# Kernel optimization log

Hardware: AMD Instinct MI355X
Metric: run time of the kernel (lower is better)

Reference implementation:

```python
import jax, jax.numpy as jnp
import numpy as np

EPS = 1e-5

def _linear(x, w, b):
    # torch nn.Linear convention: w is [out, in]
    return jnp.einsum('...i,oi->...o', x, w) + b

def _l2_normalize(x, axis=-1):
    n = jnp.sqrt(jnp.sum(x * x, axis=axis, keepdims=True))
    return x / jnp.maximum(n, 1e-12)

def _online_softmax_scan(sim):
    # sim: [B, H, L]. Running max m_t and running sum s_t = sum_{i<=t} exp(sim_i - m_t)
    def combine(a, b):
        ma, sa = a
        mb, sb = b
        m = jnp.maximum(ma, mb)
        s = sa * jnp.exp(ma - m) + sb * jnp.exp(mb - m)
        return m, s
    m_scan, s_scan = jax.lax.associative_scan(combine, (sim, jnp.ones_like(sim)), axis=2)
    return m_scan, s_scan


def setup_inputs() -> dict:
    key = jax.random.key(0)
    ks = jax.random.split(key, 8)
    B, L, D = 2, 2048, 256
    H, h = 8, 32
    s = 1.0 / np.sqrt(D)
    inp = {
        'x': jax.random.normal(ks[0], (B, L, D), jnp.float32),
        'wq_w': jax.random.normal(ks[1], (D, D), jnp.float32) * s,
        'wq_b': jnp.zeros((D,), jnp.float32),
        'wk_w': jax.random.normal(ks[2], (D, D), jnp.float32) * s,
        'wk_b': jnp.zeros((D,), jnp.float32),
        'wv_w': jax.random.normal(ks[3], (D, D), jnp.float32) * s,
        'wv_b': jnp.zeros((D,), jnp.float32),
        'wo_w': jax.random.normal(ks[4], (D, D), jnp.float32) * s,
        'wo_b': jnp.zeros((D,), jnp.float32),
        'wg_w': jax.random.normal(ks[5], (1, h * h), jnp.float32) * (1.0 / np.sqrt(h * h)),
        'wg_b': jnp.zeros((1,), jnp.float32),
        'kv_norm_scale': jnp.ones((1, H, 1, h, h), jnp.float32),
        'qk_norm_scale': jnp.full((1, H, 1), 1.0 / np.sqrt(h), jnp.float32),
    }
    return inp


def reference(x, wq_w, wq_b, wk_w, wk_b, wv_w, wv_b, wo_w, wo_b,
              wg_w, wg_b, kv_norm_scale, qk_norm_scale):
    B, L, D = x.shape
    H, h = kv_norm_scale.shape[1], kv_norm_scale.shape[3]

    q = _linear(x, wq_w, wq_b).reshape(B, L, H, h).transpose(0, 2, 1, 3)  # bhld
    k = _linear(x, wk_w, wk_b).reshape(B, L, H, h).transpose(0, 2, 1, 3)
    v = _linear(x, wv_w, wv_b).reshape(B, L, H, h).transpose(0, 2, 1, 3)

    sim = jnp.einsum('bhld,bhld->bhl', q, k) * qk_norm_scale  # [B,H,L]

    k = _l2_normalize(k)
    v = _l2_normalize(v)

    # outer-product KV state per position: [B,H,L,h,h]
    Z = jnp.einsum('bhld,bhle->bhlde', v, k) * kv_norm_scale

    # gating: squared ReLU of linear over flattened h*h features
    gate_inputs = Z.reshape(B, H, L, h * h)
    gates_logits = jnp.einsum('bhli,oi->bhlo', gate_inputs, wg_w) + wg_b  # [B,H,L,1]
    gates = jnp.square(jax.nn.relu(gates_logits)) + EPS
    gates = gates[..., None]  # [B,H,L,1,1]
    gated_Z = gates * Z

    # associative scans along L
    m_scan, s_scan = _online_softmax_scan(sim)        # [B,H,L]
    Z_scan = jnp.cumsum(gated_Z, axis=2)              # [B,H,L,h,h]
    g_scan = jnp.cumsum(gates, axis=2)                # [B,H,L,1,1]

    softmax_weights = (jnp.exp(sim - m_scan) / (s_scan + EPS))[..., None, None]
    gated_weights = Z_scan / (g_scan + EPS)
    attn_weights = gated_weights * (1.0 + jax.nn.silu(softmax_weights))

    ctxt = jnp.einsum('bhld,bhlde->bhle', q, attn_weights)
    ctxt = ctxt.transpose(0, 2, 1, 3).reshape(B, L, D)
    return _linear(ctxt, wo_w, wo_b)
```

## Files before the change

kernel.cpp:

```cpp
#include <hip/hip_runtime.h>
#include <math.h>

#define EPSV 1e-5f

static constexpr int Ls = 2048, Hh = 8;
static constexpr int NCH = 64, T = 32;

typedef unsigned short u16;
using frag  = __attribute__((ext_vector_type(8))) short;
using f32x4 = __attribute__((ext_vector_type(4))) float;

__device__ __forceinline__ void split_bf16(float v, u16& hi, u16& lo) {
    const unsigned u = __float_as_uint(v);
    hi = (u16)(u >> 16);
    const float hf = __uint_as_float((unsigned)hi << 16);
    lo = (u16)(__float_as_uint(v - hf) >> 16);
}

__device__ __forceinline__ unsigned pk2(u16 a, u16 b) {
    return (unsigned)a | ((unsigned)b << 16);
}

__device__ __forceinline__ void split8(const float4& a, const float4& b,
                                       uint4& hi, uint4& lo) {
    u16 h[8], l[8];
    const float f[8] = {a.x, a.y, a.z, a.w, b.x, b.y, b.z, b.w};
#pragma unroll
    for (int i = 0; i < 8; ++i) split_bf16(f[i], h[i], l[i]);
    hi = make_uint4(pk2(h[0], h[1]), pk2(h[2], h[3]), pk2(h[4], h[5]), pk2(h[6], h[7]));
    lo = make_uint4(pk2(l[0], l[1]), pk2(l[2], l[3]), pk2(l[4], l[5]), pk2(l[6], l[7]));
}

__global__ __launch_bounds__(256) void qkv_fused(
    const float* __restrict__ x,
    const float* __restrict__ wq, const float* __restrict__ wk, const float* __restrict__ wv,
    const float* __restrict__ bq, const float* __restrict__ bk, const float* __restrict__ bv,
    const float* __restrict__ wg_w, const float* __restrict__ wg_b,
    const float* __restrict__ kvs, const float* __restrict__ qks,
    float* __restrict__ qh, float* __restrict__ kh, float* __restrict__ vh,
    float* __restrict__ simG, float* __restrict__ gG,
    float* __restrict__ ZcT, float* __restrict__ mT, float* __restrict__ sT,
    float* __restrict__ gTt)
{
    constexpr int LDK = 40;
    constexpr int LDT = 66;
    __shared__ __align__(16) float smemf[8960];
    __shared__ float lsim[2][32], lg2[2][32];

    u16* As_hi = (u16*)smemf;
    u16* As_lo = As_hi + 1280;
    u16* Wst   = As_lo + 1280;
    float* Qt = smemf;
    float* Kt = Qt + 32 * LDT;
    float* Vt = Kt + 32 * LDT;
    float* wkS = smemf + 6336;

    const int tid = threadIdx.x;
    const int mt = blockIdx.x, nt = blockIdx.y;
    const int m0 = mt * 32, ncol0 = nt * 64;
    const int bidx = m0 >> 11, lg = m0 & (Ls - 1);
    const int cg = lg >> 5;
    const int wave = tid >> 6, lane = tid & 63;
    const int l15 = lane & 15, quad = lane >> 4;
    const int srow = tid >> 2, sk = (tid & 3) * 8;
    const int rf = wave & 1, cfp = wave >> 1;

    const float* Wsrc[3] = {wq, wk, wv};
    f32x4 acc[3][2] = {};

    float4 ca0, ca1, cw0[3], cw1[3];
    if (tid < 128) {
        ca0 = *(const float4*)&x[(size_t)(m0 + srow) * 256 + 0 + sk];
        ca1 = *(const float4*)&x[(size_t)(m0 + srow) * 256 + 0 + sk + 4];
    }
#pragma unroll
    for (int w = 0; w < 3; ++w) {
        cw0[w] = *(const float4*)&Wsrc[w][(size_t)(ncol0 + srow) * 256 + 0 + sk];
        cw1[w] = *(const float4*)&Wsrc[w][(size_t)(ncol0 + srow) * 256 + 0 + sk + 4];
    }

#pragma unroll
    for (int kk = 0; kk < 8; ++kk) {
        __syncthreads();
        {
            uint4 hi, lo;
            if (tid < 128) {
                split8(ca0, ca1, hi, lo);
                *(uint4*)&As_hi[srow * LDK + sk] = hi;
                *(uint4*)&As_lo[srow * LDK + sk] = lo;
            }
#pragma unroll
            for (int w = 0; w < 3; ++w) {
                split8(cw0[w], cw1[w], hi, lo);
                *(uint4*)&Wst[w * 5120 + srow * LDK + sk] = hi;
                *(uint4*)&Wst[w * 5120 + 2560 + srow * LDK + sk] = lo;
            }
        }
        __syncthreads();

        if (kk < 7) {
            const int k0n = (kk + 1) * 32;
            if (tid < 128) {
                ca0 = *(const float4*)&x[(size_t)(m0 + srow) * 256 + k0n + sk];
                ca1 = *(const float4*)&x[(size_t)(m0 + srow) * 256 + k0n + sk + 4];
            }
#pragma unroll
            for (int w = 0; w < 3; ++w) {
                cw0[w] = *(const float4*)&Wsrc[w][(size_t)(ncol0 + srow) * 256 + k0n + sk];
                cw1[w] = *(const float4*)&Wsrc[w][(size_t)(ncol0 + srow) * 256 + k0n + sk + 4];
            }
        }

        const frag ah = *(const frag*)&As_hi[(rf * 16 + l15) * LDK + quad * 8];
        const frag al = *(const frag*)&As_lo[(rf * 16 + l15) * LDK + quad * 8];
#pragma unroll
        for (int w = 0; w < 3; ++w)
#pragma unroll
            for (int cf = 0; cf < 2; ++cf) {
                const u16* bp = &Wst[w * 5120 + ((cfp * 2 + cf) * 16 + l15) * LDK + quad * 8];
                const frag bh = *(const frag*)bp;
                const frag bl = *(const frag*)(bp + 2560);
                acc[w][cf] = __builtin_amdgcn_mfma_f32_16x16x32_bf16(ah, bh, acc[w][cf], 0, 0, 0);
                acc[w][cf] = __builtin_amdgcn_mfma_f32_16x16x32_bf16(ah, bl, acc[w][cf], 0, 0, 0);
                acc[w][cf] = __builtin_amdgcn_mfma_f32_16x16x32_bf16(al, bh, acc[w][cf], 0, 0, 0);
            }
    }
    __syncthreads();

    {
        float* tiles[3] = {Qt, Kt, Vt};
        const float* biases[3] = {bq, bk, bv};
#pragma unroll
        for (int w = 0; w < 3; ++w)
#pragma unroll
            for (int cf = 0; cf < 2; ++cf) {
                const int col = (cfp * 2 + cf) * 16 + l15;
                const float bias = biases[w][ncol0 + col];
#pragma unroll
                for (int r = 0; r < 4; ++r) {
                    const int m = rf * 16 + quad * 4 + r;
                    tiles[w][m * LDT + col] = acc[w][cf][r] + bias;
                }
            }
        for (int i = tid; i < 2048; i += 256) {
            const int h = i >> 10, de = i & 1023;
            wkS[h * 1024 + de] = wg_w[de] * kvs[(nt * 2 + h) * 1024 + de];
        }
    }
    __syncthreads();

    {
        const int task = tid >> 2, sub = tid & 3;
        const int h = task >> 5, l = task & 31;
        const int cb = h * 32, e0 = sub * 8;
        float ksum = 0.f, vsum = 0.f, qk = 0.f;
#pragma unroll
        for (int e = e0; e < e0 + 8; ++e) {
            const float kv = Kt[l * LDT + cb + e];
            const float vv = Vt[l * LDT + cb + e];
            const float qv = Qt[l * LDT + cb + e];
            ksum = fmaf(kv, kv, ksum);
            vsum = fmaf(vv, vv, vsum);
            qk = fmaf(qv, kv, qk);
        }
        ksum += __shfl_xor(ksum, 1); ksum += __shfl_xor(ksum, 2);
        vsum += __shfl_xor(vsum, 1); vsum += __shfl_xor(vsum, 2);
        qk   += __shfl_xor(qk, 1);   qk   += __shfl_xor(qk, 2);
        const float kscale = 1.f / fmaxf(sqrtf(ksum), 1e-12f);
        const float vscale = 1.f / fmaxf(sqrtf(vsum), 1e-12f);
#pragma unroll
        for (int e = e0; e < e0 + 8; ++e) {
            Kt[l * LDT + cb + e] *= kscale;
            Vt[l * LDT + cb + e] *= vscale;
        }
        if (sub == 0) {
            const float sim = qk * qks[nt * 2 + h];
            lsim[h][l] = sim;
            simG[(size_t)(bidx * 8 + nt * 2 + h) * Ls + lg + l] = sim;
        }
    }
    __syncthreads();

    {
        const float* tl[3] = {Qt, Kt, Vt};
        float* gl[3] = {qh, kh, vh};
#pragma unroll
        for (int arr = 0; arr < 3; ++arr)
#pragma unroll
            for (int it = 0; it < 4; ++it) {
                const int idx = it * 512 + tid * 2;
                const int l = idx >> 6, col = idx & 63;
                const int h = col >> 5, e = col & 31;
                float2 v;
                v.x = tl[arr][l * LDT + h * 32 + e];
                v.y = tl[arr][l * LDT + h * 32 + e + 1];
                *(float2*)&gl[arr][(size_t)(bidx * 8 + nt * 2 + h) * 65536 +
                                   (size_t)(lg + l) * 32 + e] = v;
            }
    }

    {
        const int task = tid >> 2, sub = tid & 3;
        const int h = task >> 5, l = task & 31;
        float vreg[32];
#pragma unroll 8
        for (int d = 0; d < 32; ++d) vreg[d] = Vt[l * LDT + h * 32 + d];
        float u = 0.f;
        const int e0 = sub * 8;
#pragma unroll
        for (int e = e0; e < e0 + 8; ++e) {
            float s = 0.f;
#pragma unroll 8
            for (int d = 0; d < 32; ++d)
                s = fmaf(vreg[d], wkS[h * 1024 + d * 32 + e], s);
            u = fmaf(s, Kt[l * LDT + h * 32 + e], u);
        }
        u += __shfl_xor(u, 1);
        u += __shfl_xor(u, 2);
        if (sub == 0) {
            const float r = fmaxf(u + wg_b[0], 0.f);
            const float g = r * r + EPSV;
            lg2[h][l] = g;
            gG[(size_t)(bidx * 8 + nt * 2 + h) * Ls + lg + l] = g;
        }
    }
    __syncthreads();

    {
        const int d = tid >> 3, e0 = (tid & 7) * 4;
#pragma unroll
        for (int h = 0; h < 2; ++h) {
            float z0 = 0.f, z1 = 0.f, z2 = 0.f, z3 = 0.f;
#pragma unroll 8
            for (int l = 0; l < 32; ++l) {
                const float gv = lg2[h][l] * Vt[l * LDT + h * 32 + d];
                z0 = fmaf(gv, Kt[l * LDT + h * 32 + e0 + 0], z0);
                z1 = fmaf(gv, Kt[l * LDT + h * 32 + e0 + 1], z1);
                z2 = fmaf(gv, Kt[l * LDT + h * 32 + e0 + 2], z2);
                z3 = fmaf(gv, Kt[l * LDT + h * 32 + e0 + 3], z3);
            }
            const int bhg = bidx * 8 + nt * 2 + h;
            float4 zv; zv.x = z0; zv.y = z1; zv.z = z2; zv.w = z3;
            *(float4*)&ZcT[((size_t)bhg * NCH + cg) * 1024 + d * 32 + e0] = zv;
        }
    }

    if (wave < 2 && lane < 32) {
        const int h = wave;
        float m = lsim[h][lane], s = 1.f, g = lg2[h][lane];
#pragma unroll
        for (int off = 16; off; off >>= 1) {
            const float mo = __shfl_xor(m, off);
            const float so = __shfl_xor(s, off);
            const float mn = fmaxf(m, mo);
            s = s * __expf(m - mn) + so * __expf(mo - mn);
            m = mn;
            g += __shfl_xor(g, off);
        }
        if (lane == 0) {
            const int bhg = bidx * 8 + nt * 2 + h;
            mT[bhg * NCH + cg] = m;
            sT[bhg * NCH + cg] = s;
            gTt[bhg * NCH + cg] = g;
        }
    }
}

__global__ __launch_bounds__(256) void prefix_kernel(
    float* __restrict__ Zc, float* __restrict__ mT, float* __restrict__ sT,
    float* __restrict__ gTt,
    const float* __restrict__ kvs, float* __restrict__ aW, float* __restrict__ bW,
    int* __restrict__ flagW)
{
    const int bh = blockIdx.x, seg = blockIdx.y;
    const int tid = threadIdx.x;
    const int el = seg * 256 + tid;
    float* Zb = Zc + (size_t)bh * NCH * 1024 + el;

    float v[NCH];
#pragma unroll
    for (int i = 0; i < NCH; ++i) v[i] = Zb[(size_t)i * 1024];
    float run = 0.f;
#pragma unroll
    for (int i = 0; i < NCH; ++i) {
        const float t = v[i];
        Zb[(size_t)i * 1024] = run;
        run += t;
    }

    if (seg == 0 && tid < 64) {
        float m = mT[bh * NCH + tid], s = sT[bh * NCH + tid], g = gTt[bh * NCH + tid];
#pragma unroll
        for (int off = 1; off < 64; off <<= 1) {
            const float mo = __shfl_up(m, off);
            const float so = __shfl_up(s, off);
            const float go = __shfl_up(g, off);
            if (tid >= off) {
                const float mn = fmaxf(m, mo);
                s = s * __expf(m - mn) + so * __expf(mo - mn);
                m = mn;
                g += go;
            }
        }
        float me = __shfl_up(m, 1), se = __shfl_up(s, 1), ge = __shfl_up(g, 1);
        if (tid == 0) { me = -1e30f; se = 0.f; ge = 0.f; }
        mT[bh * NCH + tid] = me;
        sT[bh * NCH + tid] = se;
        gTt[bh * NCH + tid] = ge;
    }

    if (bh == 0 && seg == 3) {
        const int h = tid >> 5, e = tid & 31;
        const float* K = kvs + h * 1024;
        const float k00 = K[0];
        int ok = (k00 != 0.0f);
        for (int d = 0; d < 32; ++d) {
            const float lhs = K[d * 32 + e] * k00;
            const float rhs = K[d * 32] * K[e];
            const float diff = fabsf(lhs - rhs);
            if (diff > 1e-6f * fmaxf(fmaxf(fabsf(lhs), fabsf(rhs)), 1e-20f)) ok = 0;
        }
        aW[h * 32 + e] = K[e * 32];
        bW[h * 32 + e] = (k00 != 0.0f) ? K[e] / k00 : 0.f;
        const int allok = __syncthreads_and(ok);
        if (tid == 0) flagW[0] = allok;
    }
}

__global__ __launch_bounds__(1024) void chunk_out_kernel(
    const float* __restrict__ qh, const float* __restrict__ knG, const float* __restrict__ vnG,
    const float* __restrict__ simG, const float* __restrict__ gG,
    const float* __restrict__ kvs,
    const float* __restrict__ ZcP, const float* __restrict__ mP,
    const float* __restrict__ sP, const float* __restrict__ gP,
    const float* __restrict__ aW, const float* __restrict__ bW,
    const int* __restrict__ flagW,
    u16* __restrict__ chi, u16* __restrict__ clo)
{
    __shared__ float qa[1024], knb[1024], zp[1024], lkvs[1024];
    __shared__ float vnT[32 * 33], sW[32 * 33];
    __shared__ float la[32], lb[32], lg[T], lsim[T];
    const int tid = threadIdx.x;
    const int c = blockIdx.x, bh = blockIdx.y, h = bh & 7, b = bh >> 3;
    const int l = tid >> 5, lane = tid & 31;
    const size_t base = ((size_t)bh * Ls + c * T) * 32;

    const float qv = qh[base + tid];
    const float knv = knG[base + tid];
    const float vnv = vnG[base + tid];
    const float kvsv = kvs[h * 1024 + tid];
    const int flag = flagW[0];
    const float mp = mP[bh * NCH + c];
    const float sp = sP[bh * NCH + c];
    const float gp = gP[bh * NCH + c];
    vnT[lane * 33 + l] = vnv;
    zp[tid] = ZcP[((size_t)bh * NCH + c) * 1024 + tid];
    lkvs[tid] = kvsv;
    if (tid < 32) {
        la[tid] = aW[h * 32 + tid];
        lb[tid] = bW[h * 32 + tid];
        lg[tid] = gG[bh * Ls + c * T + tid];
        lsim[tid] = simG[bh * Ls + c * T + tid];
    }
    __syncthreads();

    qa[tid] = flag ? qv * la[lane] : qv;
    knb[tid] = flag ? knv * lb[lane] : knv;

    float wgt;
    {
        float mm = (lane <= l) ? lsim[lane] : -1e30f;
        float ss = (lane <= l) ? 1.f : 0.f;
        float gg = (lane <= l) ? lg[lane] : 0.f;
#pragma unroll
        for (int off = 1; off < 32; off <<= 1) {
            const float mo = __shfl_xor(mm, off);
            const float so = __shfl_xor(ss, off);
            const float go = __shfl_xor(gg, off);
            const float mn = fmaxf(mm, mo);
            ss = ss * __expf(mm - mn) + so * __expf(mo - mn);
            mm = mn;
            gg += go;
        }
        const float mn = fmaxf(mp, mm);
        const float s = sp * __expf(mp - mn) + ss * __expf(mm - mn);
        const float g = gg + gp;
        const float sw = __expf(lsim[l] - mn) / (s + EPSV);
        const float sig = 1.f / (1.f + __expf(-sw));
        wgt = (1.f + sw * sig) / (g + EPSV);
    }
    __syncthreads();

    float y;
    if (flag) {
        float s = 0.f, y0 = 0.f;
        const float4* qa4 = (const float4*)&qa[l * 32];
#pragma unroll
        for (int d4 = 0; d4 < 8; ++d4) {
            const float4 q4 = qa4[d4];
            const int d = d4 * 4;
            s = fmaf(q4.x, vnT[(d + 0) * 33 + lane], s);
            s = fmaf(q4.y, vnT[(d + 1) * 33 + lane], s);
            s = fmaf(q4.z, vnT[(d + 2) * 33 + lane], s);
            s = fmaf(q4.w, vnT[(d + 3) * 33 + lane], s);
            y0 = fmaf(q4.x, zp[(d + 0) * 32 + lane], y0);
            y0 = fmaf(q4.y, zp[(d + 1) * 32 + lane], y0);
            y0 = fmaf(q4.z, zp[(d + 2) * 32 + lane], y0);
            y0 = fmaf(q4.w, zp[(d + 3) * 32 + lane], y0);
        }
        sW[l * 33 + lane] = (lane <= l) ? lg[lane] * s : 0.f;
        __syncthreads();
        y = y0 * lb[lane];
#pragma unroll 8
        for (int j = 0; j < 32; ++j)
            y = fmaf(sW[l * 33 + j], knb[j * 32 + lane], y);
        y *= wgt;
    } else {
        float qe[32];
#pragma unroll
        for (int d = 0; d < 32; ++d)
            qe[d] = qa[l * 32 + d] * lkvs[d * 32 + lane];
        y = 0.f;
#pragma unroll
        for (int d = 0; d < 32; ++d)
            y = fmaf(qe[d], zp[d * 32 + lane], y);
        for (int j = 0; j < 32; ++j) {
            float s = 0.f;
#pragma unroll
            for (int d = 0; d < 32; ++d)
                s = fmaf(qe[d], vnT[d * 33 + j], s);
            if (j <= l) y = fmaf(lg[j] * s, knb[j * 32 + lane], y);
        }
        y *= wgt;
    }
    u16 hi, lo;
    split_bf16(y, hi, lo);
    const size_t oidx = ((size_t)(b * Ls + c * T + l)) * 256 + h * 32 + lane;
    chi[oidx] = hi;
    clo[oidx] = lo;
}

__global__ __launch_bounds__(256) void out_gemm(
    const u16* __restrict__ Ahi, const u16* __restrict__ Alo,
    const float* __restrict__ wo, const float* __restrict__ bo,
    float* __restrict__ out)
{
    constexpr int LDK = 40;
    __shared__ __align__(16) u16 As_hi[32 * LDK];
    __shared__ __align__(16) u16 As_lo[32 * LDK];
    __shared__ __align__(16) u16 Ws_hi[32 * LDK];
    __shared__ __align__(16) u16 Ws_lo[32 * LDK];

    const int tid = threadIdx.x;
    const int mt = blockIdx.x, nt = blockIdx.y;
    const int m0 = mt * 32, ncol0 = nt * 32;
    const int wave = tid >> 6, lane = tid & 63;
    const int l15 = lane & 15, quad = lane >> 4;
    const int srow = tid >> 2, sk = (tid & 3) * 8;
    const int rf = wave & 1, cf = wave >> 1;

    f32x4 acc = {};

    uint4 cah, cal;
    float4 cw0, cw1;
    if (tid < 128) {
        cah = *(const uint4*)&Ahi[(size_t)(m0 + srow) * 256 + 0 + sk];
        cal = *(const uint4*)&Alo[(size_t)(m0 + srow) * 256 + 0 + sk];
    } else {
        cw0 = *(const float4*)&wo[(size_t)(ncol0 + srow - 32) * 256 + 0 + sk];
        cw1 = *(const float4*)&wo[(size_t)(ncol0 + srow - 32) * 256 + 0 + sk + 4];
    }

#pragma unroll
    for (int kk = 0; kk < 8; ++kk) {
        __syncthreads();
        if (tid < 128) {
            *(uint4*)&As_hi[srow * LDK + sk] = cah;
            *(uint4*)&As_lo[srow * LDK + sk] = cal;
        } else {
            uint4 whi, wlo;
            split8(cw0, cw1, whi, wlo);
            *(uint4*)&Ws_hi[(srow - 32) * LDK + sk] = whi;
            *(uint4*)&Ws_lo[(srow - 32) * LDK + sk] = wlo;
        }
        __syncthreads();

        if (kk < 7) {
            const int k0n = (kk + 1) * 32;
            if (tid < 128) {
                cah = *(const uint4*)&Ahi[(size_t)(m0 + srow) * 256 + k0n + sk];
                cal = *(const uint4*)&Alo[(size_t)(m0 + srow) * 256 + k0n + sk];
            } else {
                cw0 = *(const float4*)&wo[(size_t)(ncol0 + srow - 32) * 256 + k0n + sk];
                cw1 = *(const float4*)&wo[(size_t)(ncol0 + srow - 32) * 256 + k0n + sk + 4];
            }
        }

        const frag fah = *(const frag*)&As_hi[(rf * 16 + l15) * LDK + quad * 8];
        const frag fal = *(const frag*)&As_lo[(rf * 16 + l15) * LDK + quad * 8];
        const frag fbh = *(const frag*)&Ws_hi[(cf * 16 + l15) * LDK + quad * 8];
        const frag fbl = *(const frag*)&Ws_lo[(cf * 16 + l15) * LDK + quad * 8];
        acc = __builtin_amdgcn_mfma_f32_16x16x32_bf16(fah, fbh, acc, 0, 0, 0);
        acc = __builtin_amdgcn_mfma_f32_16x16x32_bf16(fah, fbl, acc, 0, 0, 0);
        acc = __builtin_amdgcn_mfma_f32_16x16x32_bf16(fal, fbh, acc, 0, 0, 0);
    }

    {
        const int o = ncol0 + cf * 16 + l15;
        const float bias = bo[o];
#pragma unroll
        for (int r = 0; r < 4; ++r) {
            const int rm = m0 + rf * 16 + quad * 4 + r;
            out[(size_t)rm * 256 + o] = acc[r] + bias;
        }
    }
}

extern "C" void kernel_launch(void* const* d_in, const int* in_sizes, int n_in,
                              void* d_out, int out_size, void* d_ws, size_t ws_size,
                              hipStream_t stream) {
    const float* x    = (const float*)d_in[0];
    const float* wq_w = (const float*)d_in[1];
    const float* wq_b = (const float*)d_in[2];
    const float* wk_w = (const float*)d_in[3];
    const float* wk_b = (const float*)d_in[4];
    const float* wv_w = (const float*)d_in[5];
    const float* wv_b = (const float*)d_in[6];
    const float* wo_w = (const float*)d_in[7];
    const float* wo_b = (const float*)d_in[8];
    const float* wg_w = (const float*)d_in[9];
    const float* wg_b = (const float*)d_in[10];
    const float* kvs  = (const float*)d_in[11];
    const float* qks  = (const float*)d_in[12];
    float* out = (float*)d_out;

    u16* chi = (u16*)d_ws;
    u16* clo = chi + 1048576;
    float* qh   = (float*)(clo + 1048576);
    float* kh   = qh + 1048576;
    float* vh   = kh + 1048576;
    float* ZcT  = vh + 1048576;
    float* simG = ZcT + 1048576;
    float* gG   = simG + 32768;
    float* mT   = gG + 32768;
    float* sT   = mT + 1024;
    float* gTt  = sT + 1024;
    float* aW   = gTt + 1024;
    float* bW   = aW + 256;
    int* flagW  = (int*)(bW + 256);

    qkv_fused<<<dim3(128, 4), 256, 0, stream>>>(
        x, wq_w, wk_w, wv_w, wq_b, wk_b, wv_b, wg_w, wg_b, kvs, qks,
        qh, kh, vh, simG, gG, ZcT, mT, sT, gTt);
    prefix_kernel<<<dim3(16, 4), 256, 0, stream>>>(
        ZcT, mT, sT, gTt, kvs, aW, bW, flagW);
    chunk_out_kernel<<<dim3(NCH, 16), 1024, 0, stream>>>(
        qh, kh, vh, simG, gG, kvs, ZcT, mT, sT, gTt, aW, bW, flagW, chi, clo);
    out_gemm<<<dim3(128, 8), 256, 0, stream>>>(
        chi, clo, wo_w, wo_b, out);
}
```

Before: 131.9 us.

## Pre-split x and weights into bf16 hi/lo in a separate kernel

Adds a prep kernel that converts x and all four weight matrices into bf16 hi/lo pairs once, so the QKV and output GEMMs load pre-split data instead of redoing the split in every tile. This removes redundant conversion ALU work, since each weight tile was previously re-split by many blocks. The qkv kernel also writes q/k/v to global straight from registers during normalization, dropping a separate LDS readback pass. The cost is an extra kernel launch plus an extra round trip of x through memory.

Measured after the change: 155.5 us. +17.9%, slower.

```diff
diff --git a/kernel.cpp b/kernel.cpp
--- a/kernel.cpp
+++ b/kernel.cpp
@@ -31,9 +31,37 @@
     lo = make_uint4(pk2(l[0], l[1]), pk2(l[2], l[3]), pk2(l[4], l[5]), pk2(l[6], l[7]));
 }
 
+__global__ __launch_bounds__(256) void prep_split(
+    const float* __restrict__ x, const float* __restrict__ wq,
+    const float* __restrict__ wk, const float* __restrict__ wv,
+    const float* __restrict__ wo,
+    u16* __restrict__ xhi, u16* __restrict__ xlo,
+    u16* __restrict__ whi, u16* __restrict__ wlo)
+{
+    const size_t i8 = ((size_t)blockIdx.x * 256 + threadIdx.x) * 8;
+    const float* src;
+    u16 *dhi, *dlo;
+    size_t off;
+    if (i8 < 1048576) {
+        src = x; off = i8; dhi = xhi; dlo = xlo;
+    } else {
+        const size_t r = i8 - 1048576;
+        const int w = (int)(r >> 16);
+        const float* ws[4] = {wq, wk, wv, wo};
+        src = ws[w]; off = r & 65535;
+        dhi = whi + (size_t)w * 65536; dlo = wlo + (size_t)w * 65536;
+    }
+    const float4 a = *(const float4*)&src[off];
+    const float4 b = *(const float4*)&src[off + 4];
+    uint4 hi, lo;
+    split8(a, b, hi, lo);
+    *(uint4*)&dhi[off] = hi;
+    *(uint4*)&dlo[off] = lo;
+}
+
 __global__ __launch_bounds__(256) void qkv_fused(
-    const float* __restrict__ x,
-    const float* __restrict__ wq, const float* __restrict__ wk, const float* __restrict__ wv,
+    const u16* __restrict__ xhi, const u16* __restrict__ xlo,
+    const u16* __restrict__ whi, const u16* __restrict__ wlo,
     const float* __restrict__ bq, const float* __restrict__ bk, const float* __restrict__ bv,
     const float* __restrict__ wg_w, const float* __restrict__ wg_b,
     const float* __restrict__ kvs, const float* __restrict__ qks,
@@ -65,49 +93,45 @@
     const int srow = tid >> 2, sk = (tid & 3) * 8;
     const int rf = wave & 1, cfp = wave >> 1;
 
-    const float* Wsrc[3] = {wq, wk, wv};
     f32x4 acc[3][2] = {};
 
-    float4 ca0, ca1, cw0[3], cw1[3];
+    uint4 cah, cal, cwh[3], cwl[3];
     if (tid < 128) {
-        ca0 = *(const float4*)&x[(size_t)(m0 + srow) * 256 + 0 + sk];
-        ca1 = *(const float4*)&x[(size_t)(m0 + srow) * 256 + 0 + sk + 4];
+        cah = *(const uint4*)&xhi[(size_t)(m0 + srow) * 256 + 0 + sk];
+        cal = *(const uint4*)&xlo[(size_t)(m0 + srow) * 256 + 0 + sk];
     }
 #pragma unroll
     for (int w = 0; w < 3; ++w) {
-        cw0[w] = *(const float4*)&Wsrc[w][(size_t)(ncol0 + srow) * 256 + 0 + sk];
-        cw1[w] = *(const float4*)&Wsrc[w][(size_t)(ncol0 + srow) * 256 + 0 + sk + 4];
+        const size_t wb = (size_t)w * 65536 + (size_t)(ncol0 + srow) * 256 + 0 + sk;
+        cwh[w] = *(const uint4*)&whi[wb];
+        cwl[w] = *(const uint4*)&wlo[wb];
     }
 
 #pragma unroll
     for (int kk = 0; kk < 8; ++kk) {
         __syncthreads();
-        {
-            uint4 hi, lo;
-            if (tid < 128) {
-                split8(ca0, ca1, hi, lo);
-                *(uint4*)&As_hi[srow * LDK + sk] = hi;
-                *(uint4*)&As_lo[srow * LDK + sk] = lo;
-            }
-#pragma unroll
-            for (int w = 0; w < 3; ++w) {
-                split8(cw0[w], cw1[w], hi, lo);
-                *(uint4*)&Wst[w * 5120 + srow * LDK + sk] = hi;
-                *(uint4*)&Wst[w * 5120 + 2560 + srow * LDK + sk] = lo;
-            }
+        if (tid < 128) {
+            *(uint4*)&As_hi[srow * LDK + sk] = cah;
+            *(uint4*)&As_lo[srow * LDK + sk] = cal;
+        }
+#pragma unroll
+        for (int w = 0; w < 3; ++w) {
+            *(uint4*)&Wst[w * 5120 + srow * LDK + sk] = cwh[w];
+            *(uint4*)&Wst[w * 5120 + 2560 + srow * LDK + sk] = cwl[w];
         }
         __syncthreads();
 
         if (kk < 7) {
             const int k0n = (kk + 1) * 32;
             if (tid < 128) {
-                ca0 = *(const float4*)&x[(size_t)(m0 + srow) * 256 + k0n + sk];
-                ca1 = *(const float4*)&x[(size_t)(m0 + srow) * 256 + k0n + sk + 4];
+                cah = *(const uint4*)&xhi[(size_t)(m0 + srow) * 256 + k0n + sk];
+                cal = *(const uint4*)&xlo[(size_t)(m0 + srow) * 256 + k0n + sk];
             }
 #pragma unroll
             for (int w = 0; w < 3; ++w) {
-                cw0[w] = *(const float4*)&Wsrc[w][(size_t)(ncol0 + srow) * 256 + k0n + sk];
-                cw1[w] = *(const float4*)&Wsrc[w][(size_t)(ncol0 + srow) * 256 + k0n + sk + 4];
+                const size_t wb = (size_t)w * 65536 + (size_t)(ncol0 + srow) * 256 + k0n + sk;
+                cwh[w] = *(const uint4*)&whi[wb];
+                cwl[w] = *(const uint4*)&wlo[wb];
             }
         }
 
@@ -153,15 +177,16 @@
         const int task = tid >> 2, sub = tid & 3;
         const int h = task >> 5, l = task & 31;
         const int cb = h * 32, e0 = sub * 8;
+        float kv8[8], vv8[8], qv8[8];
         float ksum = 0.f, vsum = 0.f, qk = 0.f;
 #pragma unroll
-        for (int e = e0; e < e0 + 8; ++e) {
-            const float kv = Kt[l * LDT + cb + e];
-            const float vv = Vt[l * LDT + cb + e];
-            const float qv = Qt[l * LDT + cb + e];
-            ksum = fmaf(kv, kv, ksum);
-            vsum = fmaf(vv, vv, vsum);
-            qk = fmaf(qv, kv, qk);
+        for (int e = 0; e < 8; ++e) {
+            kv8[e] = Kt[l * LDT + cb + e0 + e];
+            vv8[e] = Vt[l * LDT + cb + e0 + e];
+            qv8[e] = Qt[l * LDT + cb + e0 + e];
+            ksum = fmaf(kv8[e], kv8[e], ksum);
+            vsum = fmaf(vv8[e], vv8[e], vsum);
+            qk = fmaf(qv8[e], kv8[e], qk);
         }
         ksum += __shfl_xor(ksum, 1); ksum += __shfl_xor(ksum, 2);
         vsum += __shfl_xor(vsum, 1); vsum += __shfl_xor(vsum, 2);
@@ -169,10 +194,20 @@
         const float kscale = 1.f / fmaxf(sqrtf(ksum), 1e-12f);
         const float vscale = 1.f / fmaxf(sqrtf(vsum), 1e-12f);
 #pragma unroll
-        for (int e = e0; e < e0 + 8; ++e) {
-            Kt[l * LDT + cb + e] *= kscale;
-            Vt[l * LDT + cb + e] *= vscale;
-        }
+        for (int e = 0; e < 8; ++e) {
+            kv8[e] *= kscale;
+            vv8[e] *= vscale;
+            Kt[l * LDT + cb + e0 + e] = kv8[e];
+            Vt[l * LDT + cb + e0 + e] = vv8[e];
+        }
+        const size_t gb = (size_t)(bidx * 8 + nt * 2 + h) * 65536 +
+                          (size_t)(lg + l) * 32 + e0;
+        *(float4*)&qh[gb]     = make_float4(qv8[0], qv8[1], qv8[2], qv8[3]);
+        *(float4*)&qh[gb + 4] = make_float4(qv8[4], qv8[5], qv8[6], qv8[7]);
+        *(float4*)&kh[gb]     = make_float4(kv8[0], kv8[1], kv8[2], kv8[3]);
+        *(float4*)&kh[gb + 4] = make_float4(kv8[4], kv8[5], kv8[6], kv8[7]);
+        *(float4*)&vh[gb]     = make_float4(vv8[0], vv8[1], vv8[2], vv8[3]);
+        *(float4*)&vh[gb + 4] = make_float4(vv8[4], vv8[5], vv8[6], vv8[7]);
         if (sub == 0) {
             const float sim = qk * qks[nt * 2 + h];
             lsim[h][l] = sim;
@@ -180,24 +215,6 @@
         }
     }
     __syncthreads();
-
-    {
-        const float* tl[3] = {Qt, Kt, Vt};
-        float* gl[3] = {qh, kh, vh};
-#pragma unroll
-        for (int arr = 0; arr < 3; ++arr)
-#pragma unroll
-            for (int it = 0; it < 4; ++it) {
-                const int idx = it * 512 + tid * 2;
-                const int l = idx >> 6, col = idx & 63;
-                const int h = col >> 5, e = col & 31;
-                float2 v;
-                v.x = tl[arr][l * LDT + h * 32 + e];
-                v.y = tl[arr][l * LDT + h * 32 + e + 1];
-                *(float2*)&gl[arr][(size_t)(bidx * 8 + nt * 2 + h) * 65536 +
-                                   (size_t)(lg + l) * 32 + e] = v;
-            }
-    }
 
     {
         const int task = tid >> 2, sub = tid & 3;
@@ -442,8 +459,8 @@
 
 __global__ __launch_bounds__(256) void out_gemm(
     const u16* __restrict__ Ahi, const u16* __restrict__ Alo,
-    const float* __restrict__ wo, const float* __restrict__ bo,
-    float* __restrict__ out)
+    const u16* __restrict__ whi, const u16* __restrict__ wlo,
+    const float* __restrict__ bo, float* __restrict__ out)
 {
     constexpr int LDK = 40;
     __shared__ __align__(16) u16 As_hi[32 * LDK];
@@ -461,38 +478,37 @@
 
     f32x4 acc = {};
 
-    uint4 cah, cal;
-    float4 cw0, cw1;
+    uint4 c0, c1;
     if (tid < 128) {
-        cah = *(const uint4*)&Ahi[(size_t)(m0 + srow) * 256 + 0 + sk];
-        cal = *(const uint4*)&Alo[(size_t)(m0 + srow) * 256 + 0 + sk];
+        c0 = *(const uint4*)&Ahi[(size_t)(m0 + srow) * 256 + 0 + sk];
+        c1 = *(const uint4*)&Alo[(size_t)(m0 + srow) * 256 + 0 + sk];
     } else {
-        cw0 = *(const float4*)&wo[(size_t)(ncol0 + srow - 32) * 256 + 0 + sk];
-        cw1 = *(const float4*)&wo[(size_t)(ncol0 + srow - 32) * 256 + 0 + sk + 4];
+        const size_t wb = (size_t)3 * 65536 + (size_t)(ncol0 + srow - 32) * 256 + 0 + sk;
+        c0 = *(const uint4*)&whi[wb];
+        c1 = *(const uint4*)&wlo[wb];
     }
 
 #pragma unroll
     for (int kk = 0; kk < 8; ++kk) {
         __syncthreads();
         if (tid < 128) {
-            *(uint4*)&As_hi[srow * LDK + sk] = cah;
-            *(uint4*)&As_lo[srow * LDK + sk] = cal;
+            *(uint4*)&As_hi[srow * LDK + sk] = c0;
+            *(uint4*)&As_lo[srow * LDK + sk] = c1;
         } else {
-            uint4 whi, wlo;
-            split8(cw0, cw1, whi, wlo);
-            *(uint4*)&Ws_hi[(srow - 32) * LDK + sk] = whi;
-            *(uint4*)&Ws_lo[(srow - 32) * LDK + sk] = wlo;
+            *(uint4*)&Ws_hi[(srow - 32) * LDK + sk] = c0;
+            *(uint4*)&Ws_lo[(srow - 32) * LDK + sk] = c1;
         }
         __syncthreads();
 
         if (kk < 7) {
             const int k0n = (kk + 1) * 32;
             if (tid < 128) {
-                cah = *(const uint4*)&Ahi[(size_t)(m0 + srow) * 256 + k0n + sk];
-                cal = *(const uint4*)&Alo[(size_t)(m0 + srow) * 256 + k0n + sk];
+                c0 = *(const uint4*)&Ahi[(size_t)(m0 + srow) * 256 + k0n + sk];
+                c1 = *(const uint4*)&Alo[(size_t)(m0 + srow) * 256 + k0n + sk];
             } else {
-                cw0 = *(const float4*)&wo[(size_t)(ncol0 + srow - 32) * 256 + k0n + sk];
-                cw1 = *(const float4*)&wo[(size_t)(ncol0 + srow - 32) * 256 + k0n + sk + 4];
+                const size_t wb = (size_t)3 * 65536 + (size_t)(ncol0 + srow - 32) * 256 + k0n + sk;
+                c0 = *(const uint4*)&whi[wb];
+                c1 = *(const uint4*)&wlo[wb];
             }
         }
 
@@ -548,14 +564,20 @@
     float* aW   = gTt + 1024;
     float* bW   = aW + 256;
     int* flagW  = (int*)(bW + 256);
-
+    u16* xhi = (u16*)((char*)d_ws + 24u * 1024 * 1024);
+    u16* xlo = xhi + 1048576;
+    u16* whi = xlo + 1048576;
+    u16* wlo = whi + 4 * 65536;
+
+    prep_split<<<640, 256, 0, stream>>>(
+        x, wq_w, wk_w, wv_w, wo_w, xhi, xlo, whi, wlo);
     qkv_fused<<<dim3(128, 4), 256, 0, stream>>>(
-        x, wq_w, wk_w, wv_w, wq_b, wk_b, wv_b, wg_w, wg_b, kvs, qks,
+        xhi, xlo, whi, wlo, wq_b, wk_b, wv_b, wg_w, wg_b, kvs, qks,
         qh, kh, vh, simG, gG, ZcT, mT, sT, gTt);
     prefix_kernel<<<dim3(16, 4), 256, 0, stream>>>(
         ZcT, mT, sT, gTt, kvs, aW, bW, flagW);
     chunk_out_kernel<<<dim3(NCH, 16), 1024, 0, stream>>>(
         qh, kh, vh, simG, gG, kvs, ZcT, mT, sT, gTt, aW, bW, flagW, chi, clo);
     out_gemm<<<dim3(128, 8), 256, 0, stream>>>(
-        chi, clo, wo_w, wo_b, out);
-}
+        chi, clo, whi, wlo, wo_b, out);
+}
```
